# Optimization experiments

Hardware: AMD Instinct MI355X
Metric: run time of the kernel (lower is better)

## Reference

```python
import jax, jax.numpy as jnp
import numpy as np

P = 7       # patch (window) size
H_HEADS = 8
D_HEAD = 64
SCALE = D_HEAD ** -0.5


def setup_inputs() -> dict:
    key = jax.random.key(0)
    k1, k2, k3, k4 = jax.random.split(key, 4)
    dim, inner = 256, H_HEADS * D_HEAD
    fmap = jax.random.normal(k1, (32, 56, 56, dim), dtype=jnp.float32)
    Wq = jax.random.normal(k2, (dim, inner), dtype=jnp.float32) * (dim ** -0.5)
    Wkv = jax.random.normal(k3, (dim, 2 * inner), dtype=jnp.float32) * (dim ** -0.5)
    Wo = jax.random.normal(k4, (inner, dim), dtype=jnp.float32) * (inner ** -0.5)
    bo = jnp.zeros((dim,), dtype=jnp.float32)
    return {"fmap": fmap, "Wq": Wq, "Wkv": Wkv, "Wo": Wo, "bo": bo}


def reference(fmap, Wq, Wkv, Wo, bo):
    b, X, Y, c = fmap.shape
    x, y = X // P, Y // P
    h, d = H_HEADS, D_HEAD
    # window partition: b (x p1) (y p2) c -> (b x y) p1 p2 c
    f = fmap.reshape(b, x, P, y, P, c).transpose(0, 1, 3, 2, 4, 5)
    f = f.reshape(b * x * y, P, P, c)
    # 1x1 convs == matmul over channels
    q = f @ Wq                       # (B, p, p, h*d)
    k_, v = jnp.split(f @ Wkv, 2, axis=-1)
    B = b * x * y
    pp = P * P
    def to_heads(t):  # (B,p,p,h*d) -> (B,h,pp,d)
        return t.reshape(B, pp, h, d).transpose(0, 2, 1, 3)
    q, k_, v = map(to_heads, (q, k_, v))
    dots = jnp.einsum('bhid,bhjd->bhij', q, k_) * SCALE
    attn = jax.nn.softmax(dots, axis=-1)
    out = jnp.einsum('bhij,bhjd->bhid', attn, v)      # (B,h,pp,d)
    # (b x y h) (p1 p2) d -> b (x p1) (y p2) (h d)
    out = out.reshape(b, x, y, h, P, P, d)
    out = out.transpose(0, 1, 4, 2, 5, 3, 6).reshape(b, X, Y, h * d)
    return out @ Wo + bo
```

## Files before the change

kernel.cpp:

```cpp
#include <hip/hip_runtime.h>
#include <hip/hip_bf16.h>

typedef __bf16 bf16;
typedef __bf16 bf16x4 __attribute__((ext_vector_type(4)));
typedef __bf16 bf16x8 __attribute__((ext_vector_type(8)));
typedef float f32x4 __attribute__((ext_vector_type(4)));

#define TOK 100352
#define ATT_SCALE 0.125f

#define GLOAD_LDS16(g, l)                                                        \
  __builtin_amdgcn_global_load_lds((const __attribute__((address_space(1))) void*)(g), \
                                   (__attribute__((address_space(3))) void*)(l), 16, 0, 0)

__global__ __launch_bounds__(256) void transpose_cast_k(const float* __restrict__ in,
                                                        bf16* __restrict__ out, int R, int C) {
  __shared__ float t[32][33];
  int c0 = blockIdx.x * 32, r0 = blockIdx.y * 32;
  int tx = threadIdx.x, ty = threadIdx.y;
#pragma unroll
  for (int i = ty; i < 32; i += 8)
    t[i][tx] = in[(size_t)(r0 + i) * C + c0 + tx];
  __syncthreads();
#pragma unroll
  for (int i = ty; i < 32; i += 8)
    out[(size_t)(c0 + i) * R + r0 + tx] = (bf16)t[tx][i];
}

__global__ __launch_bounds__(256) void qkvg_k(const float* __restrict__ fmap,
                                              const bf16* __restrict__ Bt,
                                              bf16* __restrict__ qkv2,
                                              bf16* __restrict__ Vtg, int wbase0) {
  __shared__ bf16 Bs[2][128 * 64];
  const int tid = threadIdx.x;
  const int lane = tid & 63, wv = tid >> 6;
  const int l15 = lane & 15, l4 = lane >> 4;
  const int g = blockIdx.x;
  const int blk = blockIdx.y;
  bf16x8 af[2][8];
  int wl[2], tt[2];
#pragma unroll
  for (int m = 0; m < 2; ++m) {
    int tokl = blk * 128 + wv * 32 + m * 16 + l15;
    int w = tokl / 49, t = tokl - w * 49;
    wl[m] = w; tt[m] = t;
    int wg = wbase0 + w;
    int p1 = t / 7, p2 = t - p1 * 7;
    const float* ab = fmap +
        (size_t)((((wg >> 6) * 56) + ((wg >> 3) & 7) * 7 + p1) * 56 + (wg & 7) * 7 + p2) * 256;
#pragma unroll
    for (int j = 0; j < 8; ++j) {
      const float* p = ab + j * 32 + l4 * 8;
      float4 f0 = *(const float4*)p;
      float4 f1 = *(const float4*)(p + 4);
      bf16x8 o;
      o[0] = (bf16)f0.x; o[1] = (bf16)f0.y; o[2] = (bf16)f0.z; o[3] = (bf16)f0.w;
      o[4] = (bf16)f1.x; o[5] = (bf16)f1.y; o[6] = (bf16)f1.z; o[7] = (bf16)f1.w;
      af[m][j] = o;
    }
  }
  const int sg = lane >> 3;
  const int scol = ((lane & 7) ^ (sg & 7)) * 8;
#define STAGE_B(tt_, buf_)                                                                   \
  do {                                                                                       \
    int bn_ = g * 4 + ((tt_) >> 2), ks_ = (tt_) & 3;                                         \
    _Pragma("unroll") for (int i_ = 0; i_ < 4; ++i_)                                         \
        GLOAD_LDS16(Bt + (size_t)(bn_ * 128 + wv * 32 + i_ * 8 + sg) * 256 + ks_ * 64 + scol,\
                    Bs[buf_] + wv * 2048 + i_ * 512);                                        \
  } while (0)

  f32x4 acc[2][8] = {};
  STAGE_B(0, 0);
  __syncthreads();
#pragma unroll
  for (int t = 0; t < 16; ++t) {
    const int cur = t & 1, ks = t & 3;
    if (t < 15) STAGE_B(t + 1, cur ^ 1);
#pragma unroll
    for (int kk = 0; kk < 2; ++kk) {
      bf16x8 bfr[8];
#pragma unroll
      for (int n = 0; n < 8; ++n) {
        int rv = n * 16 + l15;
        bfr[n] = *(const bf16x8*)((const char*)Bs[cur] +
                 ((rv * 128 + kk * 64 + l4 * 16) ^ ((rv & 7) << 4)));
      }
#pragma unroll
      for (int m = 0; m < 2; ++m)
#pragma unroll
        for (int n = 0; n < 8; ++n)
          acc[m][n] = __builtin_amdgcn_mfma_f32_16x16x32_bf16(bfr[n], af[m][ks * 2 + kk],
                                                              acc[m][n], 0, 0, 0);
    }
    if (ks == 3) {
      const int bn = g * 4 + (t >> 2);
      if (g < 2) {
#pragma unroll
        for (int m = 0; m < 2; ++m) {
          size_t row = (size_t)blk * 128 + wv * 32 + m * 16 + l15;
#pragma unroll
          for (int n = 0; n < 8; ++n) {
            bf16x4 pk;
#pragma unroll
            for (int r = 0; r < 4; ++r) pk[r] = (bf16)acc[m][n][r];
            *(bf16x4*)(qkv2 + row * 1024 + bn * 128 + n * 16 + l4 * 4) = pk;
          }
        }
      } else {
#pragma unroll
        for (int m = 0; m < 2; ++m) {
#pragma unroll
          for (int n = 0; n < 8; ++n) {
            int d0 = (bn - 8) * 128 + n * 16 + l4 * 4;
            int h = d0 >> 6, dd = d0 & 63;
            size_t vb = ((size_t)wl[m] * 8 + h) * 4096 + (size_t)dd * 64 + tt[m];
#pragma unroll
            for (int r = 0; r < 4; ++r) Vtg[vb + (size_t)r * 64] = (bf16)acc[m][n][r];
          }
        }
      }
#pragma unroll
      for (int m = 0; m < 2; ++m)
#pragma unroll
        for (int n = 0; n < 8; ++n) acc[m][n] = (f32x4){0.f, 0.f, 0.f, 0.f};
    }
    __syncthreads();
  }
#undef STAGE_B
}

__global__ __launch_bounds__(256) void attn2_k(const bf16* __restrict__ qkv2,
                                               const bf16* __restrict__ Vtg,
                                               const bf16* __restrict__ Wo_t,
                                               const float* __restrict__ bias,
                                               float* __restrict__ out, int wbase) {
  __shared__ bf16 Ks[2][64 * 64], Vt[2][64 * 64], Ps[4 * 16 * 64], HO[64 * 64];
  const int w = blockIdx.x;
  const int tid = threadIdx.x, lane = tid & 63, wv = tid >> 6;
  const int l15 = lane & 15, l4 = lane >> 4;
  const size_t bqk = (size_t)w * 49 * 1024;
  const bf16* vbase = Vtg + (size_t)w * 8 * 4096;
  const int wg = wbase + w;
  char* pbase = (char*)Ps + wv * 2048;
  const int sr = wv * 8 + (lane >> 3);
  const int scc = ((lane & 7) ^ ((lane >> 3) & 7)) * 8;
#pragma unroll
  for (int i = 0; i < 2; ++i) {
    GLOAD_LDS16(qkv2 + bqk + (size_t)(i * 32 + sr) * 1024 + 512 + scc,
                Ks[0] + i * 2048 + wv * 512);
    GLOAD_LDS16(vbase + (size_t)(i * 32 + sr) * 64 + scc, Vt[0] + i * 2048 + wv * 512);
  }
  f32x4 acco[4][4] = {};
  for (int h = 0; h < 8; ++h) {
    const int cur = h & 1;
    __syncthreads();
    if (h < 7) {
#pragma unroll
      for (int i = 0; i < 2; ++i) {
        GLOAD_LDS16(qkv2 + bqk + (size_t)(i * 32 + sr) * 1024 + 512 + (h + 1) * 64 + scc,
                    Ks[cur ^ 1] + i * 2048 + wv * 512);
        GLOAD_LDS16(vbase + (size_t)(h + 1) * 4096 + (i * 32 + sr) * 64 + scc,
                    Vt[cur ^ 1] + i * 2048 + wv * 512);
      }
    }
    const int rq = wv * 16 + l15;
    bf16x8 aq[2];
#pragma unroll
    for (int kk = 0; kk < 2; ++kk)
      aq[kk] = *(const bf16x8*)(qkv2 + bqk + (size_t)rq * 1024 + h * 64 + kk * 32 + l4 * 8);
    f32x4 s[4] = {};
#pragma unroll
    for (int kk = 0; kk < 2; ++kk) {
#pragma unroll
      for (int n = 0; n < 4; ++n) {
        int rk = n * 16 + l15;
        bf16x8 bk = *(const bf16x8*)((const char*)Ks[cur] +
                    ((rk * 128 + kk * 64 + l4 * 16) ^ ((rk & 7) << 4)));
        s[n] = __builtin_amdgcn_mfma_f32_16x16x32_bf16(aq[kk], bk, s[n], 0, 0, 0);
      }
    }
    float pr[4][4];
#pragma unroll
    for (int reg = 0; reg < 4; ++reg) {
      float m = -1e30f;
#pragma unroll
      for (int n = 0; n < 4; ++n) {
        float v = s[n][reg] * ATT_SCALE;
        if (n * 16 + l15 < 49) m = fmaxf(m, v);
      }
#pragma unroll
      for (int d = 1; d < 16; d <<= 1) m = fmaxf(m, __shfl_xor(m, d));
      float sum = 0.f;
#pragma unroll
      for (int n = 0; n < 4; ++n) {
        float p = (n * 16 + l15 < 49) ? __expf(s[n][reg] * ATT_SCALE - m) : 0.f;
        pr[n][reg] = p;
        sum += p;
      }
#pragma unroll
      for (int d = 1; d < 16; d <<= 1) sum += __shfl_xor(sum, d);
      float inv = 1.f / sum;
#pragma unroll
      for (int n = 0; n < 4; ++n) pr[n][reg] *= inv;
    }
#pragma unroll
    for (int n = 0; n < 4; ++n)
#pragma unroll
      for (int reg = 0; reg < 4; ++reg) {
        int rl = l4 * 4 + reg, col = n * 16 + l15;
        int off = ((rl * 64 + col) * 2) ^ ((rl & 7) << 4);
        *(bf16*)(pbase + off) = (bf16)pr[n][reg];
      }
    f32x4 o[4] = {};
#pragma unroll
    for (int kk = 0; kk < 2; ++kk) {
      int rp = l15;
      bf16x8 ap = *(const bf16x8*)(pbase +
                  ((rp * 128 + kk * 64 + l4 * 16) ^ ((rp & 7) << 4)));
#pragma unroll
      for (int n = 0; n < 4; ++n) {
        int rv = n * 16 + l15;
        bf16x8 bv = *(const bf16x8*)((const char*)Vt[cur] +
                    ((rv * 128 + kk * 64 + l4 * 16) ^ ((rv & 7) << 4)));
        o[n] = __builtin_amdgcn_mfma_f32_16x16x32_bf16(bv, ap, o[n], 0, 0, 0);
      }
    }
    {
      int hrow = wv * 16 + l15;
#pragma unroll
      for (int n = 0; n < 4; ++n) {
        bf16x4 pk;
#pragma unroll
        for (int r = 0; r < 4; ++r) pk[r] = (bf16)o[n][r];
        int off = (hrow * 128 + n * 32 + l4 * 8) ^ ((hrow & 7) << 4);
        *(bf16x4*)((char*)HO + off) = pk;
      }
    }
    __syncthreads();
#pragma unroll
    for (int kk = 0; kk < 2; ++kk) {
      bf16x8 af[4];
#pragma unroll
      for (int m = 0; m < 4; ++m) {
        int r = m * 16 + l15;
        af[m] = *(const bf16x8*)((const char*)HO +
                 ((r * 128 + kk * 64 + l4 * 16) ^ ((r & 7) << 4)));
      }
#pragma unroll
      for (int n = 0; n < 4; ++n) {
        int wr = wv * 64 + n * 16 + l15;
        bf16x8 bv = *(const bf16x8*)(Wo_t + (size_t)wr * 512 + h * 64 + kk * 32 + l4 * 8);
#pragma unroll
        for (int m = 0; m < 4; ++m)
          acco[m][n] = __builtin_amdgcn_mfma_f32_16x16x32_bf16(bv, af[m], acco[m][n], 0, 0, 0);
      }
    }
  }
  int bb = wg >> 6, xx = (wg >> 3) & 7, yy = wg & 7;
#pragma unroll
  for (int m = 0; m < 4; ++m) {
    int rl = m * 16 + l15;
    if (rl < 49) {
      int p1 = rl / 7, p2 = rl - p1 * 7;
      size_t orow = (size_t)(bb * 56 + xx * 7 + p1) * 56 + yy * 7 + p2;
      float* op = out + orow * 256 + wv * 64;
#pragma unroll
      for (int n = 0; n < 4; ++n) {
        int col = n * 16 + l4 * 4;
        float4 b4 = *(const float4*)(bias + wv * 64 + col);
        float4 v;
        v.x = acco[m][n][0] + b4.x;
        v.y = acco[m][n][1] + b4.y;
        v.z = acco[m][n][2] + b4.z;
        v.w = acco[m][n][3] + b4.w;
        *(float4*)(op + col) = v;
      }
    }
  }
}

extern "C" void kernel_launch(void* const* d_in, const int* in_sizes, int n_in,
                              void* d_out, int out_size, void* d_ws, size_t ws_size,
                              hipStream_t stream) {
  const float* fmap = (const float*)d_in[0];
  const float* Wq = (const float*)d_in[1];
  const float* Wkv = (const float*)d_in[2];
  const float* Wo = (const float*)d_in[3];
  const float* bo = (const float*)d_in[4];
  float* out = (float*)d_out;
  char* ws = (char*)d_ws;

  const size_t WQKV_B = 1536ull * 256 * 2;
  const size_t WO_B = 256ull * 512 * 2;
  const size_t wbytes = WQKV_B + WO_B;

  int nc = 0;
  size_t Tc = 0, VtgB = 0;
  for (int c = 2; c <= 16; c <<= 1) {
    size_t tc = TOK / c;
    size_t vb = (tc / 49) * 65536ull;
    if (wbytes + vb + tc * 2048ull + 65536ull <= ws_size) { nc = c; Tc = tc; VtgB = vb; break; }
  }
  if (nc == 0) return;

  bf16* Wqkv_t = (bf16*)(ws);
  bf16* Wo_t = (bf16*)(ws + WQKV_B);
  bf16* Vtg = (bf16*)(ws + wbytes);
  bf16* qkv2 = (bf16*)(ws + wbytes + VtgB);

  hipMemsetAsync(Vtg, 0, VtgB, stream);

  hipLaunchKernelGGL(transpose_cast_k, dim3(16, 8), dim3(32, 8), 0, stream, Wq, Wqkv_t, 256, 512);
  hipLaunchKernelGGL(transpose_cast_k, dim3(32, 8), dim3(32, 8), 0, stream, Wkv,
                     Wqkv_t + 512 * 256, 256, 1024);
  hipLaunchKernelGGL(transpose_cast_k, dim3(8, 16), dim3(32, 8), 0, stream, Wo, Wo_t, 512, 256);

  for (int c = 0; c < nc; ++c) {
    int tok0 = (int)(c * Tc);
    int wloc = (int)(Tc / 49);
    hipLaunchKernelGGL(qkvg_k, dim3(3, (int)(Tc / 128)), dim3(256), 0, stream, fmap, Wqkv_t,
                       qkv2, Vtg, tok0 / 49);
    hipLaunchKernelGGL(attn2_k, dim3(wloc), dim3(256), 0, stream, qkv2, Vtg, Wo_t, bo, out,
                       tok0 / 49);
  }
}
```

Baseline: 358.1 us.

## Replace syncthreads with vmcnt-counted raw barriers and prefetch Wo fragments

```diff
diff --git a/kernel.cpp b/kernel.cpp
--- a/kernel.cpp
+++ b/kernel.cpp
@@ -12,6 +12,10 @@
 #define GLOAD_LDS16(g, l)                                                        \
   __builtin_amdgcn_global_load_lds((const __attribute__((address_space(1))) void*)(g), \
                                    (__attribute__((address_space(3))) void*)(l), 16, 0, 0)
+#define VMCNT(n) asm volatile("s_waitcnt vmcnt(" #n ")" ::: "memory")
+#define LGKMCNT0 asm volatile("s_waitcnt lgkmcnt(0)" ::: "memory")
+#define SCHED_FENCE __builtin_amdgcn_sched_barrier(0)
+#define RAW_BARRIER __builtin_amdgcn_s_barrier()
 
 __global__ __launch_bounds__(256) void transpose_cast_k(const float* __restrict__ in,
                                                         bf16* __restrict__ out, int R, int C) {
@@ -71,11 +75,18 @@
 
   f32x4 acc[2][8] = {};
   STAGE_B(0, 0);
-  __syncthreads();
 #pragma unroll
   for (int t = 0; t < 16; ++t) {
     const int cur = t & 1, ks = t & 3;
-    if (t < 15) STAGE_B(t + 1, cur ^ 1);
+    if (t < 15) {
+      STAGE_B(t + 1, cur ^ 1);
+      VMCNT(4);
+    } else {
+      VMCNT(0);
+    }
+    SCHED_FENCE;
+    RAW_BARRIER;
+    SCHED_FENCE;
 #pragma unroll
     for (int kk = 0; kk < 2; ++kk) {
       bf16x8 bfr[8];
@@ -124,12 +135,13 @@
 #pragma unroll
         for (int n = 0; n < 8; ++n) acc[m][n] = (f32x4){0.f, 0.f, 0.f, 0.f};
     }
-    __syncthreads();
+    SCHED_FENCE;
+    RAW_BARRIER;
   }
 #undef STAGE_B
 }
 
-__global__ __launch_bounds__(256) void attn2_k(const bf16* __restrict__ qkv2,
+__global__ __launch_bounds__(256) void attn3_k(const bf16* __restrict__ qkv2,
                                                const bf16* __restrict__ Vtg,
                                                const bf16* __restrict__ Wo_t,
                                                const float* __restrict__ bias,
@@ -144,30 +156,42 @@
   char* pbase = (char*)Ps + wv * 2048;
   const int sr = wv * 8 + (lane >> 3);
   const int scc = ((lane & 7) ^ ((lane >> 3) & 7)) * 8;
-#pragma unroll
-  for (int i = 0; i < 2; ++i) {
-    GLOAD_LDS16(qkv2 + bqk + (size_t)(i * 32 + sr) * 1024 + 512 + scc,
-                Ks[0] + i * 2048 + wv * 512);
-    GLOAD_LDS16(vbase + (size_t)(i * 32 + sr) * 64 + scc, Vt[0] + i * 2048 + wv * 512);
-  }
+#define STAGE_KV(h_, buf_)                                                                \
+  do {                                                                                    \
+    _Pragma("unroll") for (int i_ = 0; i_ < 2; ++i_) {                                    \
+      GLOAD_LDS16(qkv2 + bqk + (size_t)(i_ * 32 + sr) * 1024 + 512 + (h_) * 64 + scc,     \
+                  Ks[buf_] + i_ * 2048 + wv * 512);                                       \
+      GLOAD_LDS16(vbase + (size_t)(h_) * 4096 + (i_ * 32 + sr) * 64 + scc,                \
+                  Vt[buf_] + i_ * 2048 + wv * 512);                                       \
+    }                                                                                     \
+  } while (0)
+  STAGE_KV(0, 0);
   f32x4 acco[4][4] = {};
+#pragma unroll
   for (int h = 0; h < 8; ++h) {
     const int cur = h & 1;
-    __syncthreads();
-    if (h < 7) {
-#pragma unroll
-      for (int i = 0; i < 2; ++i) {
-        GLOAD_LDS16(qkv2 + bqk + (size_t)(i * 32 + sr) * 1024 + 512 + (h + 1) * 64 + scc,
-                    Ks[cur ^ 1] + i * 2048 + wv * 512);
-        GLOAD_LDS16(vbase + (size_t)(h + 1) * 4096 + (i * 32 + sr) * 64 + scc,
-                    Vt[cur ^ 1] + i * 2048 + wv * 512);
-      }
-    }
     const int rq = wv * 16 + l15;
     bf16x8 aq[2];
 #pragma unroll
     for (int kk = 0; kk < 2; ++kk)
       aq[kk] = *(const bf16x8*)(qkv2 + bqk + (size_t)rq * 1024 + h * 64 + kk * 32 + l4 * 8);
+    bf16x8 wo[4][2];
+#pragma unroll
+    for (int n = 0; n < 4; ++n)
+#pragma unroll
+      for (int kk = 0; kk < 2; ++kk)
+        wo[n][kk] = *(const bf16x8*)(Wo_t + (size_t)(wv * 64 + n * 16 + l15) * 512 + h * 64 +
+                                     kk * 32 + l4 * 8);
+    SCHED_FENCE;
+    if (h < 7) {
+      STAGE_KV(h + 1, cur ^ 1);
+      VMCNT(4);
+    } else {
+      VMCNT(0);
+    }
+    SCHED_FENCE;
+    RAW_BARRIER;
+    SCHED_FENCE;
     f32x4 s[4] = {};
 #pragma unroll
     for (int kk = 0; kk < 2; ++kk) {
@@ -236,7 +260,10 @@
         *(bf16x4*)((char*)HO + off) = pk;
       }
     }
-    __syncthreads();
+    LGKMCNT0;
+    SCHED_FENCE;
+    RAW_BARRIER;
+    SCHED_FENCE;
 #pragma unroll
     for (int kk = 0; kk < 2; ++kk) {
       bf16x8 af[4];
@@ -247,15 +274,14 @@
                  ((r * 128 + kk * 64 + l4 * 16) ^ ((r & 7) << 4)));
       }
 #pragma unroll
-      for (int n = 0; n < 4; ++n) {
-        int wr = wv * 64 + n * 16 + l15;
-        bf16x8 bv = *(const bf16x8*)(Wo_t + (size_t)wr * 512 + h * 64 + kk * 32 + l4 * 8);
+      for (int n = 0; n < 4; ++n)
 #pragma unroll
         for (int m = 0; m < 4; ++m)
-          acco[m][n] = __builtin_amdgcn_mfma_f32_16x16x32_bf16(bv, af[m], acco[m][n], 0, 0, 0);
-      }
-    }
-  }
+          acco[m][n] = __builtin_amdgcn_mfma_f32_16x16x32_bf16(wo[n][kk], af[m], acco[m][n],
+                                                               0, 0, 0);
+    }
+  }
+#undef STAGE_KV
   int bb = wg >> 6, xx = (wg >> 3) & 7, yy = wg & 7;
 #pragma unroll
   for (int m = 0; m < 4; ++m) {
@@ -320,7 +346,7 @@
     int wloc = (int)(Tc / 49);
     hipLaunchKernelGGL(qkvg_k, dim3(3, (int)(Tc / 128)), dim3(256), 0, stream, fmap, Wqkv_t,
                        qkv2, Vtg, tok0 / 49);
-    hipLaunchKernelGGL(attn2_k, dim3(wloc), dim3(256), 0, stream, qkv2, Vtg, Wo_t, bo, out,
+    hipLaunchKernelGGL(attn3_k, dim3(wloc), dim3(256), 0, stream, qkv2, Vtg, Wo_t, bo, out,
                        tok0 / 49);
   }
 }
```

New measurement: 372.8 us. 4.1% more time.
